# Performance work log

Hardware: AMD Instinct MI355X
Metric: run time of the kernel (lower is better)

The kernel has to match this reference:

```python
import jax, jax.numpy as jnp
import numpy as np
from jax import lax

G = 32          # growthrate / num_features
KS = 3          # filter_size
PAD = (KS - 1) // 2
NUM_LAYERS = 4


def _conv2d(x, w, b):
    # x: [B, Cin, H, W], w: [Cout, Cin, k, k]
    y = lax.conv_general_dilated(
        x, w, window_strides=(1, 1), padding=[(PAD, PAD), (PAD, PAD)],
        dimension_numbers=("NCHW", "OIHW", "NCHW"))
    return y + b[None, :, None, None]


def _scan_cell(xs, w, b):
    # xs: [T, B, Cin, H, W]; ConvLSTM-like cell: A = tanh(conv(cat(x, c)))
    # split A -> (ai[G], af[G], ao[1]); h = ai; c_next = sigmoid(ao) * af
    T, B, _, H, W = xs.shape
    c0 = jnp.zeros((B, G, H, W), xs.dtype)

    def step(c, x):
        A = jnp.tanh(_conv2d(jnp.concatenate([x, c], axis=1), w, b))
        h = A[:, :G]
        cand = A[:, G:2 * G]
        gate = jax.nn.sigmoid(A[:, 2 * G:])
        c_next = gate * cand
        return c_next, (h, c_next, gate)

    _, (hs, cs, gs) = lax.scan(step, c0, xs)
    return hs, cs, gs  # each [T, B, G or 1, H, W]


def setup_inputs() -> dict:
    key = jax.random.key(0)
    ks = jax.random.split(key, 1 + 4 * NUM_LAYERS)
    T, B, C, H, W = 8, 4, 32, 64, 64
    inp = {"x": jax.random.normal(ks[0], (T, B, C, H, W), jnp.float32)}
    cin = [C] + [2 * l * G for l in range(1, NUM_LAYERS)]  # [32, 64, 128, 192]
    cout = 2 * G + 1
    for l in range(NUM_LAYERS):
        ci = cin[l] + G
        inp[f"wf{l}"] = jax.random.normal(ks[1 + 4 * l], (cout, ci, KS, KS), jnp.float32) * 0.02
        inp[f"bf{l}"] = jax.random.normal(ks[2 + 4 * l], (cout,), jnp.float32) * 0.02
        inp[f"wb{l}"] = jax.random.normal(ks[3 + 4 * l], (cout, ci, KS, KS), jnp.float32) * 0.02
        inp[f"bb{l}"] = jax.random.normal(ks[4 + 4 * l], (cout,), jnp.float32) * 0.02
    return inp


def reference(x, wf0, bf0, wb0, bb0, wf1, bf1, wb1, bb1,
              wf2, bf2, wb2, bb2, wf3, bf3, wb3, bb3):
    fwd = [(wf0, bf0), (wf1, bf1), (wf2, bf2), (wf3, bf3)]
    bwd = [(wb0, bb0), (wb1, bb1), (wb2, bb2), (wb3, bb3)]
    output = x  # [T, B, C, H, W]
    lr_h, lr_c, lr_g = [], [], []
    for l in range(NUM_LAYERS):
        hf, cf, gf = _scan_cell(output, *fwd[l])
        hb, _, _ = _scan_cell(output[::-1], *bwd[l])
        hb = hb[::-1]  # align backward pass to original time order
        cur = jnp.concatenate([hf, hb], axis=2)  # [T, B, 2G, H, W]
        output = cur if l == 0 else jnp.concatenate([output, cur], axis=2)
        lr_h.append(hf[-1]); lr_c.append(cf[-1]); lr_g.append(gf[-1])
    return (output, jnp.stack(lr_h), jnp.stack(lr_c), jnp.stack(lr_g))
```

## Files before the change

### kernel.cpp

```cpp
#include <hip/hip_runtime.h>
#include <math.h>

#define T_STEPS 8
#define HW 4096
#define XSTR 192
#define FR_ROW 4352

typedef unsigned short u16;
typedef __attribute__((ext_vector_type(8))) short short8;
typedef __attribute__((ext_vector_type(4))) short short4v;
typedef __attribute__((ext_vector_type(4))) float f32x4;

__device__ __forceinline__ u16 f2bf(float f) {
    unsigned u = __builtin_bit_cast(unsigned, f);
    u += 0x7fffu + ((u >> 16) & 1u);
    return (u16)(u >> 16);
}
__device__ __forceinline__ float bf2f(u16 h) {
    unsigned u = ((unsigned)h) << 16;
    return __builtin_bit_cast(float, u);
}
__device__ __forceinline__ float ftanh(float x) {
    float e = __expf(2.f * x);
    return 1.f - 2.f * __builtin_amdgcn_rcpf(e + 1.f);
}
__device__ __forceinline__ float fsigm(float x) {
    return __builtin_amdgcn_rcpf(1.f + __expf(-x));
}

__global__ __launch_bounds__(256) void transpose_halo(
    const float* __restrict__ src, u16* __restrict__ XT, int src_ctot)
{
    __shared__ float tile[32][257];
    const int img = blockIdx.z;
    const int px0 = blockIdx.x * 256;
    const float* s = src + (size_t)img * src_ctot * HW + px0;
    #pragma unroll
    for (int c = 0; c < 32; ++c)
        tile[c][threadIdx.x] = s[(size_t)c * HW + threadIdx.x];
    __syncthreads();
    const int c = threadIdx.x & 31, pb = threadIdx.x >> 5;
    const int r0 = px0 >> 6;
    for (int p = pb; p < 256; p += 8) {
        int row = r0 + (p >> 6), col = p & 63;
        XT[((size_t)img * 4356 + (row + 1) * 66 + col + 1) * XSTR + c] = f2bf(tile[c][p]);
    }
}

__global__ __launch_bounds__(256) void prep_w(
    const float* __restrict__ wf, const float* __restrict__ wb,
    u16* __restrict__ Wr, int ci_total)
{
    int idx = blockIdx.x * 256 + threadIdx.x;
    int total = 2 * 9 * 80 * ci_total;
    if (idx >= total) return;
    int ci = idx % ci_total;
    int rest = idx / ci_total;
    int co = rest % 80; rest /= 80;
    int tap = rest % 9;
    int dir = rest / 9;
    const float* w = dir ? wb : wf;
    float v = (co < 65) ? w[((size_t)co * ci_total + ci) * 9 + tap] : 0.f;
    Wr[idx] = f2bf(v);
}

__global__ __launch_bounds__(512, 2) void convx_mfma(
    const u16* __restrict__ XT, const u16* __restrict__ Wr,
    const float* __restrict__ b_f, const float* __restrict__ b_b,
    u16* __restrict__ convx, int cin, int ci_total)
{
    __shared__ u16 xs[6 * 66 * 32];
    const int tid = threadIdx.x;
    const int l = tid & 63, wv = tid >> 6;
    const int g = l >> 4, ln16 = l & 15;
    const int img = blockIdx.z;
    const int dir = wv & 1;
    const int wrow = wv >> 1;
    const int r0  = blockIdx.x * 4;
    const int orow = r0 + wrow;

    const float* bias = dir ? b_b : b_f;
    f32x4 acc[5][4];
    #pragma unroll
    for (int mt = 0; mt < 5; ++mt)
        #pragma unroll
        for (int r = 0; r < 4; ++r) {
            int co = mt * 16 + g * 4 + r;
            float bv = (co < 65) ? bias[co] : 0.f;
            #pragma unroll
            for (int nt = 0; nt < 4; ++nt) acc[mt][nt][r] = bv;
        }

    const u16* wdir = Wr + (size_t)dir * 9 * 80 * ci_total + g * 8;
    const u16* xim  = XT + (size_t)img * 4356 * XSTR;

    for (int ch = 0; ch < cin; ch += 32) {
        __syncthreads();
        #pragma unroll
        for (int k = 0; k < 4; ++k) {
            int idx = k * 512 + tid;
            if (idx < 1584) {
                int seg = idx & 3;
                int pr  = idx >> 2;
                short8 v = *(const short8*)(xim + (size_t)(r0 * 66 + pr) * XSTR + ch + seg * 8);
                *(short8*)(xs + (size_t)idx * 8) = v;
            }
        }
        __syncthreads();

        #pragma unroll
        for (int ky = 0; ky < 3; ++ky) {
            #pragma unroll
            for (int kx = 0; kx < 3; ++kx) {
                const int tap = ky * 3 + kx;
                const u16* xb = xs + ((size_t)((wrow + ky) * 66 + ln16 + kx)) * 32 + g * 8;
                short8 bv0 = *(const short8*)(xb);
                short8 bv1 = *(const short8*)(xb + 16 * 32);
                short8 bv2 = *(const short8*)(xb + 32 * 32);
                short8 bv3 = *(const short8*)(xb + 48 * 32);
                const u16* wb_ = wdir + ((size_t)tap * 80 + ln16) * ci_total + ch;
                #pragma unroll
                for (int mt = 0; mt < 5; ++mt) {
                    short8 af = *(const short8*)(wb_ + (size_t)mt * 16 * ci_total);
                    acc[mt][0] = __builtin_amdgcn_mfma_f32_16x16x32_bf16(af, bv0, acc[mt][0], 0, 0, 0);
                    acc[mt][1] = __builtin_amdgcn_mfma_f32_16x16x32_bf16(af, bv1, acc[mt][1], 0, 0, 0);
                    acc[mt][2] = __builtin_amdgcn_mfma_f32_16x16x32_bf16(af, bv2, acc[mt][2], 0, 0, 0);
                    acc[mt][3] = __builtin_amdgcn_mfma_f32_16x16x32_bf16(af, bv3, acc[mt][3], 0, 0, 0);
                }
            }
        }
    }

    const int zimg = dir * 32 + img;
    u16* cb = convx + ((size_t)zimg * 64 + orow) * FR_ROW;
    #pragma unroll
    for (int mt = 0; mt < 4; ++mt)
        #pragma unroll
        for (int nt = 0; nt < 4; ++nt) {
            short4v pk;
            #pragma unroll
            for (int r = 0; r < 4; ++r) pk[r] = (short)f2bf(acc[mt][nt][r]);
            *(short4v*)(cb + (size_t)(nt * 4 + mt) * 256 + l * 4) = pk;
        }
    if (g == 0) {
        #pragma unroll
        for (int nt = 0; nt < 4; ++nt) {
            short4v pk;
            #pragma unroll
            for (int r = 0; r < 4; ++r) pk[r] = (short)f2bf(acc[4][nt][r]);
            *(short4v*)(cb + 4096 + nt * 64 + ln16 * 4) = pk;
        }
    }
}

__global__ __launch_bounds__(256) void rec_mfma(
    const u16* __restrict__ cT_in, u16* __restrict__ cT_out,
    const u16* __restrict__ Wr, const u16* __restrict__ convx,
    float* __restrict__ out_t,
    float* __restrict__ lrh, float* __restrict__ lrc, float* __restrict__ lrg,
    u16* __restrict__ XT,
    int cin, int ci_total, int layer, int step)
{
    const int tid = threadIdx.x;
    const int l = tid & 63, wv = tid >> 6;
    const int g = l >> 4, ln16 = l & 15;
    const int z = blockIdx.z;
    const int dir = z >> 2, b = z & 3;
    const int t = dir ? (7 - step) : step;
    const int row  = blockIdx.x * 2 + (wv >> 1);
    const int nb   = (wv & 1) * 2;
    const int col0 = nb * 16;

    const int zimg = dir * 32 + t * 4 + b;
    const u16* cxb = convx + ((size_t)zimg * 64 + row) * FR_ROW;
    f32x4 acc[5][2];
    #pragma unroll
    for (int mt = 0; mt < 4; ++mt)
        #pragma unroll
        for (int nt = 0; nt < 2; ++nt) {
            short4v pk = *(const short4v*)(cxb + (size_t)((nb + nt) * 4 + mt) * 256 + l * 4);
            #pragma unroll
            for (int r = 0; r < 4; ++r) acc[mt][nt][r] = bf2f((u16)pk[r]);
        }
    #pragma unroll
    for (int nt = 0; nt < 2; ++nt) {
        if (g == 0) {
            short4v pk = *(const short4v*)(cxb + 4096 + (nb + nt) * 64 + ln16 * 4);
            #pragma unroll
            for (int r = 0; r < 4; ++r) acc[4][nt][r] = bf2f((u16)pk[r]);
        } else {
            #pragma unroll
            for (int r = 0; r < 4; ++r) acc[4][nt][r] = 0.f;
        }
    }

    const u16* wdir = Wr + (size_t)dir * 9 * 80 * ci_total + cin + g * 8;
    const u16* cim  = cT_in + (size_t)z * 4356 * 32 + g * 8;

    #pragma unroll
    for (int ky = 0; ky < 3; ++ky) {
        #pragma unroll
        for (int kx = 0; kx < 3; ++kx) {
            const int tap = ky * 3 + kx;
            const u16* xb_ = cim + (size_t)((row + ky) * 66 + col0 + ln16 + kx) * 32;
            short8 bv0 = *(const short8*)(xb_);
            short8 bv1 = *(const short8*)(xb_ + 16 * 32);
            const u16* wb_ = wdir + ((size_t)tap * 80 + ln16) * ci_total;
            #pragma unroll
            for (int mt = 0; mt < 5; ++mt) {
                short8 af = *(const short8*)(wb_ + (size_t)mt * 16 * ci_total);
                acc[mt][0] = __builtin_amdgcn_mfma_f32_16x16x32_bf16(af, bv0, acc[mt][0], 0, 0, 0);
                acc[mt][1] = __builtin_amdgcn_mfma_f32_16x16x32_bf16(af, bv1, acc[mt][1], 0, 0, 0);
            }
        }
    }

    const bool last_f = (dir == 0) && (step == 7);
    float val[2], gv[2];
    #pragma unroll
    for (int nt = 0; nt < 2; ++nt) {
        val[nt] = fsigm(ftanh(acc[4][nt][0]));
        gv[nt]  = __shfl(val[nt], ln16);
    }

    const size_t obase = (size_t)(t * 4 + b) * 256 + 64 * layer + dir * 32;
    const int chb = 64 * layer + dir * 32;
    #pragma unroll
    for (int mt = 0; mt < 2; ++mt)
        #pragma unroll
        for (int nt = 0; nt < 2; ++nt) {
            int px = row * 64 + col0 + nt * 16 + ln16;
            short4v pkh;
            #pragma unroll
            for (int r = 0; r < 4; ++r) {
                int co = mt * 16 + g * 4 + r;
                float v = ftanh(acc[mt][nt][r]);
                out_t[(obase + co) * HW + px] = v;
                pkh[r] = (short)f2bf(v);
                if (last_f) lrh[((size_t)(layer * 4 + b) * 32 + co) * HW + px] = v;
            }
            if (layer < 3)
                *(short4v*)(XT + ((size_t)(t * 4 + b) * 4356 + (row + 1) * 66 +
                                  (col0 + nt * 16 + ln16 + 1)) * XSTR + chb + mt * 16 + g * 4) = pkh;
        }
    #pragma unroll
    for (int mt = 2; mt < 4; ++mt)
        #pragma unroll
        for (int nt = 0; nt < 2; ++nt) {
            short4v pk;
            #pragma unroll
            for (int r = 0; r < 4; ++r) {
                int k = (mt - 2) * 16 + g * 4 + r;
                float c = gv[nt] * ftanh(acc[mt][nt][r]);
                pk[r] = (short)f2bf(c);
                if (last_f)
                    lrc[((size_t)(layer * 4 + b) * 32 + k) * HW + row * 64 + col0 + nt * 16 + ln16] = c;
            }
            int colh = col0 + nt * 16 + ln16 + 1;
            *(short4v*)(cT_out + ((size_t)z * 4356 + (row + 1) * 66 + colh) * 32 + (mt - 2) * 16 + g * 4) = pk;
        }
    if (last_f && g == 0) {
        #pragma unroll
        for (int nt = 0; nt < 2; ++nt)
            lrg[(size_t)(layer * 4 + b) * HW + row * 64 + col0 + nt * 16 + ln16] = val[nt];
    }
}

extern "C" void kernel_launch(void* const* d_in, const int* in_sizes, int n_in,
                              void* d_out, int out_size, void* d_ws, size_t ws_size,
                              hipStream_t stream)
{
    const float* x = (const float*)d_in[0];
    float* out = (float*)d_out;
    float* lrh = out + (size_t)33554432;
    float* lrc = lrh + (size_t)2097152;
    float* lrg = lrc + (size_t)2097152;

    char* ws = (char*)d_ws;
    u16* convx = (u16*)ws;
    size_t off = 35651584 + 4096;
    u16* cT_a = (u16*)(ws + off); off += 2230272;
    u16* cT_b = (u16*)(ws + off); off += 2230272;
    u16* XT   = (u16*)(ws + off); off += 53526528;
    u16* Wr   = (u16*)(ws + off);

    hipMemsetAsync(XT, 0, 53526528, stream);
    hipMemsetAsync(cT_b, 0, 2230272, stream);
    transpose_halo<<<dim3(16, 1, 32), 256, 0, stream>>>(x, XT, 32);

    for (int l = 0; l < 4; ++l) {
        const float* wf = (const float*)d_in[1 + 4 * l];
        const float* bf = (const float*)d_in[2 + 4 * l];
        const float* wb = (const float*)d_in[3 + 4 * l];
        const float* bb = (const float*)d_in[4 + 4 * l];
        int cin = (l == 0) ? 32 : 64 * l;
        int ci_total = cin + 32;

        prep_w<<<dim3((2 * 9 * 80 * ci_total + 255) / 256), 256, 0, stream>>>(wf, wb, Wr, ci_total);
        convx_mfma<<<dim3(16, 1, 32), 512, 0, stream>>>(XT, Wr, bf, bb, convx, cin, ci_total);

        hipMemsetAsync(cT_a, 0, 2230272, stream);
        for (int s = 0; s < 8; ++s) {
            const u16* cin_p = (s & 1) ? cT_b : cT_a;
            u16* cout_p      = (s & 1) ? cT_a : cT_b;
            rec_mfma<<<dim3(32, 1, 8), 256, 0, stream>>>(
                cin_p, cout_p, Wr, convx, out, lrh, lrc, lrg, XT, cin, ci_total, l, s);
        }
    }
}
```

Measured before the change: 616.4 us.

## Fuse two recurrent timesteps per launch with halo recompute and async LDS staging

The recurrent kernel now runs two consecutive timesteps per launch. The first step is computed for the block's rows plus one halo row on each side, and its cell state is kept in shared memory for the second step. This halves the number of serial recurrent launches and cuts a global round trip of the cell state, in exchange for redundant halo-row computation and larger blocks. The input convolution also switches to double-buffered direct global-to-LDS loads so the next channel chunk is fetched while the current one feeds MFMA, which drops one barrier per chunk.

```diff
diff --git a/kernel.cpp b/kernel.cpp
--- a/kernel.cpp
+++ b/kernel.cpp
@@ -26,6 +26,11 @@
 }
 __device__ __forceinline__ float fsigm(float x) {
     return __builtin_amdgcn_rcpf(1.f + __expf(-x));
+}
+__device__ __forceinline__ void gload_lds16(const u16* g, u16* lds) {
+    __builtin_amdgcn_global_load_lds(
+        (const __attribute__((address_space(1))) unsigned*)g,
+        (__attribute__((address_space(3))) unsigned*)lds, 16, 0, 0);
 }
 
 __global__ __launch_bounds__(256) void transpose_halo(
@@ -69,7 +74,7 @@
     const float* __restrict__ b_f, const float* __restrict__ b_b,
     u16* __restrict__ convx, int cin, int ci_total)
 {
-    __shared__ u16 xs[6 * 66 * 32];
+    __shared__ u16 xs[2][16384];
     const int tid = threadIdx.x;
     const int l = tid & 63, wv = tid >> 6;
     const int g = l >> 4, ln16 = l & 15;
@@ -94,31 +99,35 @@
     const u16* wdir = Wr + (size_t)dir * 9 * 80 * ci_total + g * 8;
     const u16* xim  = XT + (size_t)img * 4356 * XSTR;
 
-    for (int ch = 0; ch < cin; ch += 32) {
+#define STAGE(buf, chv)                                                         \
+    {                                                                           \
+        _Pragma("unroll")                                                       \
+        for (int k = 0; k < 4; ++k) {                                           \
+            int idx = k * 512 + tid;                                            \
+            if (idx < 1584)                                                     \
+                gload_lds16(xim + (size_t)(r0 * 66 + (idx >> 2)) * XSTR + (chv) \
+                            + (idx & 3) * 8,                                    \
+                            &xs[buf][(size_t)idx * 8]);                         \
+        }                                                                       \
+    }
+
+    const int nch = cin >> 5;
+    int cur = 0;
+    STAGE(0, 0)
+    for (int ch = 0; ch < nch; ++ch) {
         __syncthreads();
-        #pragma unroll
-        for (int k = 0; k < 4; ++k) {
-            int idx = k * 512 + tid;
-            if (idx < 1584) {
-                int seg = idx & 3;
-                int pr  = idx >> 2;
-                short8 v = *(const short8*)(xim + (size_t)(r0 * 66 + pr) * XSTR + ch + seg * 8);
-                *(short8*)(xs + (size_t)idx * 8) = v;
-            }
-        }
-        __syncthreads();
-
+        if (ch + 1 < nch) STAGE(cur ^ 1, (ch + 1) * 32)
         #pragma unroll
         for (int ky = 0; ky < 3; ++ky) {
             #pragma unroll
             for (int kx = 0; kx < 3; ++kx) {
                 const int tap = ky * 3 + kx;
-                const u16* xb = xs + ((size_t)((wrow + ky) * 66 + ln16 + kx)) * 32 + g * 8;
+                const u16* xb = xs[cur] + ((size_t)((wrow + ky) * 66 + ln16 + kx)) * 32 + g * 8;
                 short8 bv0 = *(const short8*)(xb);
                 short8 bv1 = *(const short8*)(xb + 16 * 32);
                 short8 bv2 = *(const short8*)(xb + 32 * 32);
                 short8 bv3 = *(const short8*)(xb + 48 * 32);
-                const u16* wb_ = wdir + ((size_t)tap * 80 + ln16) * ci_total + ch;
+                const u16* wb_ = wdir + ((size_t)tap * 80 + ln16) * ci_total + ch * 32;
                 #pragma unroll
                 for (int mt = 0; mt < 5; ++mt) {
                     short8 af = *(const short8*)(wb_ + (size_t)mt * 16 * ci_total);
@@ -129,7 +138,9 @@
                 }
             }
         }
-    }
+        cur ^= 1;
+    }
+#undef STAGE
 
     const int zimg = dir * 32 + img;
     u16* cb = convx + ((size_t)zimg * 64 + orow) * FR_ROW;
@@ -153,116 +164,219 @@
     }
 }
 
-__global__ __launch_bounds__(256) void rec_mfma(
+__global__ __launch_bounds__(512) void rec2_mfma(
     const u16* __restrict__ cT_in, u16* __restrict__ cT_out,
     const u16* __restrict__ Wr, const u16* __restrict__ convx,
     float* __restrict__ out_t,
     float* __restrict__ lrh, float* __restrict__ lrc, float* __restrict__ lrg,
     u16* __restrict__ XT,
-    int cin, int ci_total, int layer, int step)
+    int cin, int ci_total, int layer, int s0)
 {
+    __shared__ u16 cls[4 * 4 * 66 * 8];
     const int tid = threadIdx.x;
-    const int l = tid & 63, wv = tid >> 6;
+    const int l = tid & 63, w = tid >> 6;
     const int g = l >> 4, ln16 = l & 15;
+    const int rb = blockIdx.x;
     const int z = blockIdx.z;
     const int dir = z >> 2, b = z & 3;
-    const int t = dir ? (7 - step) : step;
-    const int row  = blockIdx.x * 2 + (wv >> 1);
-    const int nb   = (wv & 1) * 2;
+    const int hf = w & 1;
+    const int nb = hf * 2;
     const int col0 = nb * 16;
-
-    const int zimg = dir * 32 + t * 4 + b;
-    const u16* cxb = convx + ((size_t)zimg * 64 + row) * FR_ROW;
-    f32x4 acc[5][2];
-    #pragma unroll
-    for (int mt = 0; mt < 4; ++mt)
+    const int row0 = rb * 2;
+
+    for (int i = tid; i < 8448; i += 512) cls[i] = 0;
+    __syncthreads();
+
+    const u16* wdir = Wr + (size_t)dir * 9 * 80 * ci_total + cin + g * 8;
+
+    {
+        const int rowA = row0 + (w >> 1) - 1;
+        const int lrA  = w >> 1;
+        if ((unsigned)rowA < 64u) {
+            const int t = dir ? (7 - s0) : s0;
+            const int zimg = dir * 32 + t * 4 + b;
+            const u16* cxb = convx + ((size_t)zimg * 64 + rowA) * FR_ROW;
+            f32x4 acc[5][2];
+            #pragma unroll
+            for (int mt = 0; mt < 4; ++mt)
+                #pragma unroll
+                for (int nt = 0; nt < 2; ++nt) {
+                    short4v pk = *(const short4v*)(cxb + (size_t)((nb + nt) * 4 + mt) * 256 + l * 4);
+                    #pragma unroll
+                    for (int r = 0; r < 4; ++r) acc[mt][nt][r] = bf2f((u16)pk[r]);
+                }
+            #pragma unroll
+            for (int nt = 0; nt < 2; ++nt) {
+                if (g == 0) {
+                    short4v pk = *(const short4v*)(cxb + 4096 + (nb + nt) * 64 + ln16 * 4);
+                    #pragma unroll
+                    for (int r = 0; r < 4; ++r) acc[4][nt][r] = bf2f((u16)pk[r]);
+                } else {
+                    #pragma unroll
+                    for (int r = 0; r < 4; ++r) acc[4][nt][r] = 0.f;
+                }
+            }
+
+            const u16* cim = cT_in + (size_t)z * 4356 * 32 + g * 8;
+            #pragma unroll
+            for (int ky = 0; ky < 3; ++ky) {
+                #pragma unroll
+                for (int kx = 0; kx < 3; ++kx) {
+                    const int tap = ky * 3 + kx;
+                    const u16* xb_ = cim + (size_t)((rowA + ky) * 66 + col0 + ln16 + kx) * 32;
+                    short8 bv0 = *(const short8*)(xb_);
+                    short8 bv1 = *(const short8*)(xb_ + 16 * 32);
+                    #pragma unroll
+                    for (int mt = 0; mt < 5; ++mt) {
+                        short8 af = *(const short8*)(wdir + ((size_t)tap * 80 + ln16) * ci_total
+                                                     + (size_t)mt * 16 * ci_total);
+                        acc[mt][0] = __builtin_amdgcn_mfma_f32_16x16x32_bf16(af, bv0, acc[mt][0], 0, 0, 0);
+                        acc[mt][1] = __builtin_amdgcn_mfma_f32_16x16x32_bf16(af, bv1, acc[mt][1], 0, 0, 0);
+                    }
+                }
+            }
+
+            float val[2], gv[2];
+            #pragma unroll
+            for (int nt = 0; nt < 2; ++nt) {
+                val[nt] = fsigm(ftanh(acc[4][nt][0]));
+                gv[nt]  = __shfl(val[nt], ln16);
+            }
+
+            const bool owned = (rowA >= row0) && (rowA < row0 + 2);
+            if (owned) {
+                const size_t obase = (size_t)(t * 4 + b) * 256 + 64 * layer + dir * 32;
+                const int chb = 64 * layer + dir * 32;
+                #pragma unroll
+                for (int mt = 0; mt < 2; ++mt)
+                    #pragma unroll
+                    for (int nt = 0; nt < 2; ++nt) {
+                        int px = rowA * 64 + col0 + nt * 16 + ln16;
+                        short4v pkh;
+                        #pragma unroll
+                        for (int r = 0; r < 4; ++r) {
+                            int co = mt * 16 + g * 4 + r;
+                            float v = ftanh(acc[mt][nt][r]);
+                            out_t[(obase + co) * HW + px] = v;
+                            pkh[r] = (short)f2bf(v);
+                        }
+                        if (layer < 3)
+                            *(short4v*)(XT + ((size_t)(t * 4 + b) * 4356 + (rowA + 1) * 66 +
+                                              (col0 + nt * 16 + ln16 + 1)) * XSTR + chb + mt * 16 + g * 4) = pkh;
+                    }
+            }
+            #pragma unroll
+            for (int mt = 2; mt < 4; ++mt)
+                #pragma unroll
+                for (int nt = 0; nt < 2; ++nt) {
+                    short4v pk;
+                    #pragma unroll
+                    for (int r = 0; r < 4; ++r)
+                        pk[r] = (short)f2bf(gv[nt] * ftanh(acc[mt][nt][r]));
+                    int colh = col0 + nt * 16 + ln16 + 1;
+                    int J = (mt - 2) * 2 + (g >> 1);
+                    *(short4v*)(cls + ((size_t)((J * 4 + lrA) * 66 + colh)) * 8 + (g & 1) * 4) = pk;
+                }
+        }
+    }
+    __syncthreads();
+
+    if (w < 4) {
+        const int s1 = s0 + 1;
+        const int rowB = row0 + (w >> 1);
+        const int t = dir ? (7 - s1) : s1;
+        const int zimg = dir * 32 + t * 4 + b;
+        const u16* cxb = convx + ((size_t)zimg * 64 + rowB) * FR_ROW;
+        f32x4 acc[5][2];
+        #pragma unroll
+        for (int mt = 0; mt < 4; ++mt)
+            #pragma unroll
+            for (int nt = 0; nt < 2; ++nt) {
+                short4v pk = *(const short4v*)(cxb + (size_t)((nb + nt) * 4 + mt) * 256 + l * 4);
+                #pragma unroll
+                for (int r = 0; r < 4; ++r) acc[mt][nt][r] = bf2f((u16)pk[r]);
+            }
         #pragma unroll
         for (int nt = 0; nt < 2; ++nt) {
-            short4v pk = *(const short4v*)(cxb + (size_t)((nb + nt) * 4 + mt) * 256 + l * 4);
-            #pragma unroll
-            for (int r = 0; r < 4; ++r) acc[mt][nt][r] = bf2f((u16)pk[r]);
-        }
-    #pragma unroll
-    for (int nt = 0; nt < 2; ++nt) {
-        if (g == 0) {
-            short4v pk = *(const short4v*)(cxb + 4096 + (nb + nt) * 64 + ln16 * 4);
-            #pragma unroll
-            for (int r = 0; r < 4; ++r) acc[4][nt][r] = bf2f((u16)pk[r]);
-        } else {
-            #pragma unroll
-            for (int r = 0; r < 4; ++r) acc[4][nt][r] = 0.f;
-        }
-    }
-
-    const u16* wdir = Wr + (size_t)dir * 9 * 80 * ci_total + cin + g * 8;
-    const u16* cim  = cT_in + (size_t)z * 4356 * 32 + g * 8;
-
-    #pragma unroll
-    for (int ky = 0; ky < 3; ++ky) {
-        #pragma unroll
-        for (int kx = 0; kx < 3; ++kx) {
-            const int tap = ky * 3 + kx;
-            const u16* xb_ = cim + (size_t)((row + ky) * 66 + col0 + ln16 + kx) * 32;
-            short8 bv0 = *(const short8*)(xb_);
-            short8 bv1 = *(const short8*)(xb_ + 16 * 32);
-            const u16* wb_ = wdir + ((size_t)tap * 80 + ln16) * ci_total;
-            #pragma unroll
-            for (int mt = 0; mt < 5; ++mt) {
-                short8 af = *(const short8*)(wb_ + (size_t)mt * 16 * ci_total);
-                acc[mt][0] = __builtin_amdgcn_mfma_f32_16x16x32_bf16(af, bv0, acc[mt][0], 0, 0, 0);
-                acc[mt][1] = __builtin_amdgcn_mfma_f32_16x16x32_bf16(af, bv1, acc[mt][1], 0, 0, 0);
-            }
-        }
-    }
-
-    const bool last_f = (dir == 0) && (step == 7);
-    float val[2], gv[2];
-    #pragma unroll
-    for (int nt = 0; nt < 2; ++nt) {
-        val[nt] = fsigm(ftanh(acc[4][nt][0]));
-        gv[nt]  = __shfl(val[nt], ln16);
-    }
-
-    const size_t obase = (size_t)(t * 4 + b) * 256 + 64 * layer + dir * 32;
-    const int chb = 64 * layer + dir * 32;
-    #pragma unroll
-    for (int mt = 0; mt < 2; ++mt)
+            if (g == 0) {
+                short4v pk = *(const short4v*)(cxb + 4096 + (nb + nt) * 64 + ln16 * 4);
+                #pragma unroll
+                for (int r = 0; r < 4; ++r) acc[4][nt][r] = bf2f((u16)pk[r]);
+            } else {
+                #pragma unroll
+                for (int r = 0; r < 4; ++r) acc[4][nt][r] = 0.f;
+            }
+        }
+
+        #pragma unroll
+        for (int ky = 0; ky < 3; ++ky) {
+            #pragma unroll
+            for (int kx = 0; kx < 3; ++kx) {
+                const int tap = ky * 3 + kx;
+                const int lrB = (w >> 1) + ky;
+                const int colv = col0 + ln16 + kx;
+                const u16* xb_ = cls + ((size_t)((g * 4 + lrB) * 66 + colv)) * 8;
+                short8 bv0 = *(const short8*)(xb_);
+                short8 bv1 = *(const short8*)(xb_ + 128);
+                #pragma unroll
+                for (int mt = 0; mt < 5; ++mt) {
+                    short8 af = *(const short8*)(wdir + ((size_t)tap * 80 + ln16) * ci_total
+                                                 + (size_t)mt * 16 * ci_total);
+                    acc[mt][0] = __builtin_amdgcn_mfma_f32_16x16x32_bf16(af, bv0, acc[mt][0], 0, 0, 0);
+                    acc[mt][1] = __builtin_amdgcn_mfma_f32_16x16x32_bf16(af, bv1, acc[mt][1], 0, 0, 0);
+                }
+            }
+        }
+
+        const bool last_f = (dir == 0) && (s1 == 7);
+        float val[2], gv[2];
         #pragma unroll
         for (int nt = 0; nt < 2; ++nt) {
-            int px = row * 64 + col0 + nt * 16 + ln16;
-            short4v pkh;
-            #pragma unroll
-            for (int r = 0; r < 4; ++r) {
-                int co = mt * 16 + g * 4 + r;
-                float v = ftanh(acc[mt][nt][r]);
-                out_t[(obase + co) * HW + px] = v;
-                pkh[r] = (short)f2bf(v);
-                if (last_f) lrh[((size_t)(layer * 4 + b) * 32 + co) * HW + px] = v;
-            }
-            if (layer < 3)
-                *(short4v*)(XT + ((size_t)(t * 4 + b) * 4356 + (row + 1) * 66 +
-                                  (col0 + nt * 16 + ln16 + 1)) * XSTR + chb + mt * 16 + g * 4) = pkh;
-        }
-    #pragma unroll
-    for (int mt = 2; mt < 4; ++mt)
-        #pragma unroll
-        for (int nt = 0; nt < 2; ++nt) {
-            short4v pk;
-            #pragma unroll
-            for (int r = 0; r < 4; ++r) {
-                int k = (mt - 2) * 16 + g * 4 + r;
-                float c = gv[nt] * ftanh(acc[mt][nt][r]);
-                pk[r] = (short)f2bf(c);
-                if (last_f)
-                    lrc[((size_t)(layer * 4 + b) * 32 + k) * HW + row * 64 + col0 + nt * 16 + ln16] = c;
-            }
-            int colh = col0 + nt * 16 + ln16 + 1;
-            *(short4v*)(cT_out + ((size_t)z * 4356 + (row + 1) * 66 + colh) * 32 + (mt - 2) * 16 + g * 4) = pk;
-        }
-    if (last_f && g == 0) {
-        #pragma unroll
-        for (int nt = 0; nt < 2; ++nt)
-            lrg[(size_t)(layer * 4 + b) * HW + row * 64 + col0 + nt * 16 + ln16] = val[nt];
+            val[nt] = fsigm(ftanh(acc[4][nt][0]));
+            gv[nt]  = __shfl(val[nt], ln16);
+        }
+
+        const size_t obase = (size_t)(t * 4 + b) * 256 + 64 * layer + dir * 32;
+        const int chb = 64 * layer + dir * 32;
+        #pragma unroll
+        for (int mt = 0; mt < 2; ++mt)
+            #pragma unroll
+            for (int nt = 0; nt < 2; ++nt) {
+                int px = rowB * 64 + col0 + nt * 16 + ln16;
+                short4v pkh;
+                #pragma unroll
+                for (int r = 0; r < 4; ++r) {
+                    int co = mt * 16 + g * 4 + r;
+                    float v = ftanh(acc[mt][nt][r]);
+                    out_t[(obase + co) * HW + px] = v;
+                    pkh[r] = (short)f2bf(v);
+                    if (last_f) lrh[((size_t)(layer * 4 + b) * 32 + co) * HW + px] = v;
+                }
+                if (layer < 3)
+                    *(short4v*)(XT + ((size_t)(t * 4 + b) * 4356 + (rowB + 1) * 66 +
+                                      (col0 + nt * 16 + ln16 + 1)) * XSTR + chb + mt * 16 + g * 4) = pkh;
+            }
+        #pragma unroll
+        for (int mt = 2; mt < 4; ++mt)
+            #pragma unroll
+            for (int nt = 0; nt < 2; ++nt) {
+                short4v pk;
+                #pragma unroll
+                for (int r = 0; r < 4; ++r) {
+                    int k = (mt - 2) * 16 + g * 4 + r;
+                    float c = gv[nt] * ftanh(acc[mt][nt][r]);
+                    pk[r] = (short)f2bf(c);
+                    if (last_f)
+                        lrc[((size_t)(layer * 4 + b) * 32 + k) * HW + rowB * 64 + col0 + nt * 16 + ln16] = c;
+                }
+                int colh = col0 + nt * 16 + ln16 + 1;
+                *(short4v*)(cT_out + ((size_t)z * 4356 + (rowB + 1) * 66 + colh) * 32 + (mt - 2) * 16 + g * 4) = pk;
+            }
+        if (last_f && g == 0) {
+            #pragma unroll
+            for (int nt = 0; nt < 2; ++nt)
+                lrg[(size_t)(layer * 4 + b) * HW + rowB * 64 + col0 + nt * 16 + ln16] = val[nt];
+        }
     }
 }
 
@@ -279,13 +393,16 @@
     char* ws = (char*)d_ws;
     u16* convx = (u16*)ws;
     size_t off = 35651584 + 4096;
-    u16* cT_a = (u16*)(ws + off); off += 2230272;
-    u16* cT_b = (u16*)(ws + off); off += 2230272;
-    u16* XT   = (u16*)(ws + off); off += 53526528;
-    u16* Wr   = (u16*)(ws + off);
+    u16* cT[3];
+    cT[0] = (u16*)(ws + off); off += 2230272;
+    cT[1] = (u16*)(ws + off); off += 2230272;
+    cT[2] = (u16*)(ws + off); off += 2230272;
+    u16* XT = (u16*)(ws + off); off += 53526528;
+    u16* Wr = (u16*)(ws + off);
 
     hipMemsetAsync(XT, 0, 53526528, stream);
-    hipMemsetAsync(cT_b, 0, 2230272, stream);
+    hipMemsetAsync(cT[1], 0, 2230272, stream);
+    hipMemsetAsync(cT[2], 0, 2230272, stream);
     transpose_halo<<<dim3(16, 1, 32), 256, 0, stream>>>(x, XT, 32);
 
     for (int l = 0; l < 4; ++l) {
@@ -299,12 +416,11 @@
         prep_w<<<dim3((2 * 9 * 80 * ci_total + 255) / 256), 256, 0, stream>>>(wf, wb, Wr, ci_total);
         convx_mfma<<<dim3(16, 1, 32), 512, 0, stream>>>(XT, Wr, bf, bb, convx, cin, ci_total);
 
-        hipMemsetAsync(cT_a, 0, 2230272, stream);
-        for (int s = 0; s < 8; ++s) {
-            const u16* cin_p = (s & 1) ? cT_b : cT_a;
-            u16* cout_p      = (s & 1) ? cT_a : cT_b;
-            rec_mfma<<<dim3(32, 1, 8), 256, 0, stream>>>(
-                cin_p, cout_p, Wr, convx, out, lrh, lrc, lrg, XT, cin, ci_total, l, s);
-        }
-    }
-}
+        hipMemsetAsync(cT[0], 0, 2230272, stream);
+        for (int p = 0; p < 4; ++p) {
+            rec2_mfma<<<dim3(32, 1, 8), 512, 0, stream>>>(
+                cT[p % 3], cT[(p + 1) % 3], Wr, convx, out, lrh, lrc, lrg, XT,
+                cin, ci_total, l, 2 * p);
+        }
+    }
+}
```

After: 734.2 us. +19.1%, slower.

## Fuse eight recurrent steps into one kernel with halo recompute in LDS

Applied to the files above, without the earlier changes.

Replaces the eight per-step recurrent launches with a single kernel per layer. Each block owns two rows and recomputes a shrinking halo of neighbouring rows, so the cell state stays in double-buffered LDS and never makes a round trip through global memory. The four per-layer weight-prep launches are also merged into one upfront launch. This removes many launches and global syncs, at the cost of redundant MFMA work on halo rows (up to 16 rows per block at the first step) and higher LDS use per block.

```diff
diff --git a/kernel.cpp b/kernel.cpp
--- a/kernel.cpp
+++ b/kernel.cpp
@@ -47,19 +47,24 @@
     }
 }
 
-__global__ __launch_bounds__(256) void prep_w(
-    const float* __restrict__ wf, const float* __restrict__ wb,
-    u16* __restrict__ Wr, int ci_total)
+struct WP { const float* p[8]; };
+
+__global__ __launch_bounds__(256) void prep_w_all(WP wp, u16* __restrict__ Wr)
 {
     int idx = blockIdx.x * 256 + threadIdx.x;
-    int total = 2 * 9 * 80 * ci_total;
-    if (idx >= total) return;
-    int ci = idx % ci_total;
-    int rest = idx / ci_total;
+    if (idx >= 783360) return;
+    const int offs[5] = {0, 92160, 230400, 460800, 783360};
+    const int cit[4]  = {64, 96, 160, 224};
+    int lay = 0;
+    while (idx >= offs[lay + 1]) ++lay;
+    int li = idx - offs[lay];
+    int ci_total = cit[lay];
+    int ci = li % ci_total;
+    int rest = li / ci_total;
     int co = rest % 80; rest /= 80;
     int tap = rest % 9;
     int dir = rest / 9;
-    const float* w = dir ? wb : wf;
+    const float* w = wp.p[lay * 2 + dir];
     float v = (co < 65) ? w[((size_t)co * ci_total + ci) * 9 + tap] : 0.f;
     Wr[idx] = f2bf(v);
 }
@@ -153,116 +158,147 @@
     }
 }
 
-__global__ __launch_bounds__(256) void rec_mfma(
-    const u16* __restrict__ cT_in, u16* __restrict__ cT_out,
+__global__ __launch_bounds__(512, 2) void rec8_mfma(
     const u16* __restrict__ Wr, const u16* __restrict__ convx,
-    float* __restrict__ out_t,
-    float* __restrict__ lrh, float* __restrict__ lrc, float* __restrict__ lrg,
-    u16* __restrict__ XT,
-    int cin, int ci_total, int layer, int step)
-{
+    float* __restrict__ out_t, float* __restrict__ lrh,
+    float* __restrict__ lrc, float* __restrict__ lrg,
+    u16* __restrict__ XT, int cin, int ci_total, int layer)
+{
+    __shared__ u16 cls[2][4 * 16 * 66 * 8];
     const int tid = threadIdx.x;
-    const int l = tid & 63, wv = tid >> 6;
+    const int l = tid & 63, w = tid >> 6;
     const int g = l >> 4, ln16 = l & 15;
-    const int z = blockIdx.z;
+    const int bid = blockIdx.x;
+    const int rb = bid >> 3, z = bid & 7;
     const int dir = z >> 2, b = z & 3;
-    const int t = dir ? (7 - step) : step;
-    const int row  = blockIdx.x * 2 + (wv >> 1);
-    const int nb   = (wv & 1) * 2;
-    const int col0 = nb * 16;
-
-    const int zimg = dir * 32 + t * 4 + b;
-    const u16* cxb = convx + ((size_t)zimg * 64 + row) * FR_ROW;
-    f32x4 acc[5][2];
-    #pragma unroll
-    for (int mt = 0; mt < 4; ++mt)
-        #pragma unroll
-        for (int nt = 0; nt < 2; ++nt) {
-            short4v pk = *(const short4v*)(cxb + (size_t)((nb + nt) * 4 + mt) * 256 + l * 4);
-            #pragma unroll
-            for (int r = 0; r < 4; ++r) acc[mt][nt][r] = bf2f((u16)pk[r]);
-        }
-    #pragma unroll
-    for (int nt = 0; nt < 2; ++nt) {
-        if (g == 0) {
-            short4v pk = *(const short4v*)(cxb + 4096 + (nb + nt) * 64 + ln16 * 4);
-            #pragma unroll
-            for (int r = 0; r < 4; ++r) acc[4][nt][r] = bf2f((u16)pk[r]);
-        } else {
-            #pragma unroll
-            for (int r = 0; r < 4; ++r) acc[4][nt][r] = 0.f;
-        }
-    }
+    const int r0 = rb * 2;
+
+    {
+        short8 zz = {0, 0, 0, 0, 0, 0, 0, 0};
+        short8* f = (short8*)&cls[0][0];
+        for (int i = tid; i < 8448; i += 512) f[i] = zz;
+    }
+    __syncthreads();
 
     const u16* wdir = Wr + (size_t)dir * 9 * 80 * ci_total + cin + g * 8;
-    const u16* cim  = cT_in + (size_t)z * 4356 * 32 + g * 8;
-
-    #pragma unroll
-    for (int ky = 0; ky < 3; ++ky) {
-        #pragma unroll
-        for (int kx = 0; kx < 3; ++kx) {
-            const int tap = ky * 3 + kx;
-            const u16* xb_ = cim + (size_t)((row + ky) * 66 + col0 + ln16 + kx) * 32;
-            short8 bv0 = *(const short8*)(xb_);
-            short8 bv1 = *(const short8*)(xb_ + 16 * 32);
-            const u16* wb_ = wdir + ((size_t)tap * 80 + ln16) * ci_total;
-            #pragma unroll
-            for (int mt = 0; mt < 5; ++mt) {
-                short8 af = *(const short8*)(wb_ + (size_t)mt * 16 * ci_total);
-                acc[mt][0] = __builtin_amdgcn_mfma_f32_16x16x32_bf16(af, bv0, acc[mt][0], 0, 0, 0);
-                acc[mt][1] = __builtin_amdgcn_mfma_f32_16x16x32_bf16(af, bv1, acc[mt][1], 0, 0, 0);
-            }
-        }
-    }
-
-    const bool last_f = (dir == 0) && (step == 7);
-    float val[2], gv[2];
-    #pragma unroll
-    for (int nt = 0; nt < 2; ++nt) {
-        val[nt] = fsigm(ftanh(acc[4][nt][0]));
-        gv[nt]  = __shfl(val[nt], ln16);
-    }
-
-    const size_t obase = (size_t)(t * 4 + b) * 256 + 64 * layer + dir * 32;
-    const int chb = 64 * layer + dir * 32;
-    #pragma unroll
-    for (int mt = 0; mt < 2; ++mt)
-        #pragma unroll
-        for (int nt = 0; nt < 2; ++nt) {
-            int px = row * 64 + col0 + nt * 16 + ln16;
-            short4v pkh;
-            #pragma unroll
-            for (int r = 0; r < 4; ++r) {
-                int co = mt * 16 + g * 4 + r;
-                float v = ftanh(acc[mt][nt][r]);
-                out_t[(obase + co) * HW + px] = v;
-                pkh[r] = (short)f2bf(v);
-                if (last_f) lrh[((size_t)(layer * 4 + b) * 32 + co) * HW + px] = v;
-            }
-            if (layer < 3)
-                *(short4v*)(XT + ((size_t)(t * 4 + b) * 4356 + (row + 1) * 66 +
-                                  (col0 + nt * 16 + ln16 + 1)) * XSTR + chb + mt * 16 + g * 4) = pkh;
-        }
-    #pragma unroll
-    for (int mt = 2; mt < 4; ++mt)
-        #pragma unroll
-        for (int nt = 0; nt < 2; ++nt) {
-            short4v pk;
-            #pragma unroll
-            for (int r = 0; r < 4; ++r) {
-                int k = (mt - 2) * 16 + g * 4 + r;
-                float c = gv[nt] * ftanh(acc[mt][nt][r]);
-                pk[r] = (short)f2bf(c);
-                if (last_f)
-                    lrc[((size_t)(layer * 4 + b) * 32 + k) * HW + row * 64 + col0 + nt * 16 + ln16] = c;
-            }
-            int colh = col0 + nt * 16 + ln16 + 1;
-            *(short4v*)(cT_out + ((size_t)z * 4356 + (row + 1) * 66 + colh) * 32 + (mt - 2) * 16 + g * 4) = pk;
-        }
-    if (last_f && g == 0) {
-        #pragma unroll
-        for (int nt = 0; nt < 2; ++nt)
-            lrg[(size_t)(layer * 4 + b) * HW + row * 64 + col0 + nt * 16 + ln16] = val[nt];
+
+    #pragma unroll 1
+    for (int p = 0; p < 8; ++p) {
+        u16* wlds        = cls[p & 1];
+        const u16* rlds  = cls[(p & 1) ^ 1];
+        const int t = dir ? (7 - p) : p;
+        const int zimg = dir * 32 + t * 4 + b;
+        const int rlo = r0 - 7 + p;
+        const int ntasks = (16 - 2 * p) * 2;
+        const bool last_f = (dir == 0) && (p == 7);
+
+        #pragma unroll 1
+        for (int task = w; task < ntasks; task += 8) {
+            const int rowA = rlo + (task >> 1);
+            if ((unsigned)rowA >= 64u) continue;
+            const int nb2 = (task & 1) * 2;
+            const int col0 = nb2 * 16;
+
+            const u16* cxb = convx + ((size_t)zimg * 64 + rowA) * FR_ROW;
+            f32x4 acc[5][2];
+            #pragma unroll
+            for (int mt = 0; mt < 4; ++mt)
+                #pragma unroll
+                for (int nt = 0; nt < 2; ++nt) {
+                    short4v pk = *(const short4v*)(cxb + (size_t)((nb2 + nt) * 4 + mt) * 256 + l * 4);
+                    #pragma unroll
+                    for (int r = 0; r < 4; ++r) acc[mt][nt][r] = bf2f((u16)pk[r]);
+                }
+            #pragma unroll
+            for (int nt = 0; nt < 2; ++nt) {
+                if (g == 0) {
+                    short4v pk = *(const short4v*)(cxb + 4096 + (nb2 + nt) * 64 + ln16 * 4);
+                    #pragma unroll
+                    for (int r = 0; r < 4; ++r) acc[4][nt][r] = bf2f((u16)pk[r]);
+                } else {
+                    #pragma unroll
+                    for (int r = 0; r < 4; ++r) acc[4][nt][r] = 0.f;
+                }
+            }
+
+            if (p > 0) {
+                #pragma unroll
+                for (int ky = 0; ky < 3; ++ky) {
+                    #pragma unroll
+                    for (int kx = 0; kx < 3; ++kx) {
+                        const int tap = ky * 3 + kx;
+                        const int lr = rowA - r0 + 6 + ky;
+                        const int colv = col0 + ln16 + kx;
+                        const u16* xb_ = rlds + ((size_t)((g * 16 + lr) * 66 + colv)) * 8;
+                        short8 bv0 = *(const short8*)(xb_);
+                        short8 bv1 = *(const short8*)(xb_ + 128);
+                        #pragma unroll
+                        for (int mt = 0; mt < 5; ++mt) {
+                            short8 af = *(const short8*)(wdir + ((size_t)tap * 80 + ln16) * ci_total
+                                                         + (size_t)mt * 16 * ci_total);
+                            acc[mt][0] = __builtin_amdgcn_mfma_f32_16x16x32_bf16(af, bv0, acc[mt][0], 0, 0, 0);
+                            acc[mt][1] = __builtin_amdgcn_mfma_f32_16x16x32_bf16(af, bv1, acc[mt][1], 0, 0, 0);
+                        }
+                    }
+                }
+            }
+
+            float val[2], gv[2];
+            #pragma unroll
+            for (int nt = 0; nt < 2; ++nt) {
+                val[nt] = fsigm(ftanh(acc[4][nt][0]));
+                gv[nt]  = __shfl(val[nt], ln16);
+            }
+
+            const bool owned = (rowA >= r0) && (rowA < r0 + 2);
+            if (owned) {
+                const size_t obase = (size_t)(t * 4 + b) * 256 + 64 * layer + dir * 32;
+                const int chb = 64 * layer + dir * 32;
+                #pragma unroll
+                for (int mt = 0; mt < 2; ++mt)
+                    #pragma unroll
+                    for (int nt = 0; nt < 2; ++nt) {
+                        int px = rowA * 64 + col0 + nt * 16 + ln16;
+                        short4v pkh;
+                        #pragma unroll
+                        for (int r = 0; r < 4; ++r) {
+                            int co = mt * 16 + g * 4 + r;
+                            float v = ftanh(acc[mt][nt][r]);
+                            out_t[(obase + co) * HW + px] = v;
+                            pkh[r] = (short)f2bf(v);
+                            if (last_f) lrh[((size_t)(layer * 4 + b) * 32 + co) * HW + px] = v;
+                        }
+                        if (layer < 3)
+                            *(short4v*)(XT + ((size_t)(t * 4 + b) * 4356 + (rowA + 1) * 66 +
+                                              (col0 + nt * 16 + ln16 + 1)) * XSTR + chb + mt * 16 + g * 4) = pkh;
+                    }
+                if (last_f && g == 0) {
+                    #pragma unroll
+                    for (int nt = 0; nt < 2; ++nt)
+                        lrg[(size_t)(layer * 4 + b) * HW + rowA * 64 + col0 + nt * 16 + ln16] = val[nt];
+                }
+            }
+
+            const int lrW = rowA - r0 + 7;
+            #pragma unroll
+            for (int mt = 2; mt < 4; ++mt)
+                #pragma unroll
+                for (int nt = 0; nt < 2; ++nt) {
+                    short4v pk;
+                    #pragma unroll
+                    for (int r = 0; r < 4; ++r) {
+                        int k = (mt - 2) * 16 + g * 4 + r;
+                        float cval = gv[nt] * ftanh(acc[mt][nt][r]);
+                        pk[r] = (short)f2bf(cval);
+                        if (last_f && owned)
+                            lrc[((size_t)(layer * 4 + b) * 32 + k) * HW + rowA * 64 + col0 + nt * 16 + ln16] = cval;
+                    }
+                    int colh = col0 + nt * 16 + ln16 + 1;
+                    int J = (mt - 2) * 2 + (g >> 1);
+                    *(short4v*)(wlds + ((size_t)((J * 16 + lrW) * 66 + colh)) * 8 + (g & 1) * 4) = pk;
+                }
+        }
+        __syncthreads();
     }
 }
 
@@ -279,32 +315,30 @@
     char* ws = (char*)d_ws;
     u16* convx = (u16*)ws;
     size_t off = 35651584 + 4096;
-    u16* cT_a = (u16*)(ws + off); off += 2230272;
-    u16* cT_b = (u16*)(ws + off); off += 2230272;
-    u16* XT   = (u16*)(ws + off); off += 53526528;
-    u16* Wr   = (u16*)(ws + off);
+    u16* XT = (u16*)(ws + off); off += 53526528;
+    u16* Wr = (u16*)(ws + off);
+
+    static const int offs[4] = {0, 92160, 230400, 460800};
 
     hipMemsetAsync(XT, 0, 53526528, stream);
-    hipMemsetAsync(cT_b, 0, 2230272, stream);
     transpose_halo<<<dim3(16, 1, 32), 256, 0, stream>>>(x, XT, 32);
 
+    WP wp;
     for (int l = 0; l < 4; ++l) {
-        const float* wf = (const float*)d_in[1 + 4 * l];
+        wp.p[l * 2]     = (const float*)d_in[1 + 4 * l];
+        wp.p[l * 2 + 1] = (const float*)d_in[3 + 4 * l];
+    }
+    prep_w_all<<<dim3((783360 + 255) / 256), 256, 0, stream>>>(wp, Wr);
+
+    for (int l = 0; l < 4; ++l) {
         const float* bf = (const float*)d_in[2 + 4 * l];
-        const float* wb = (const float*)d_in[3 + 4 * l];
         const float* bb = (const float*)d_in[4 + 4 * l];
         int cin = (l == 0) ? 32 : 64 * l;
         int ci_total = cin + 32;
-
-        prep_w<<<dim3((2 * 9 * 80 * ci_total + 255) / 256), 256, 0, stream>>>(wf, wb, Wr, ci_total);
-        convx_mfma<<<dim3(16, 1, 32), 512, 0, stream>>>(XT, Wr, bf, bb, convx, cin, ci_total);
-
-        hipMemsetAsync(cT_a, 0, 2230272, stream);
-        for (int s = 0; s < 8; ++s) {
-            const u16* cin_p = (s & 1) ? cT_b : cT_a;
-            u16* cout_p      = (s & 1) ? cT_a : cT_b;
-            rec_mfma<<<dim3(32, 1, 8), 256, 0, stream>>>(
-                cin_p, cout_p, Wr, convx, out, lrh, lrc, lrg, XT, cin, ci_total, l, s);
-        }
-    }
-}
+        const u16* Wrl = Wr + offs[l];
+
+        convx_mfma<<<dim3(16, 1, 32), 512, 0, stream>>>(XT, Wrl, bf, bb, convx, cin, ci_total);
+        rec8_mfma<<<dim3(256), 512, 0, stream>>>(
+            Wrl, convx, out, lrh, lrc, lrg, XT, cin, ci_total, l);
+    }
+}
```

Result: slower. 771.0 us (+25.1%).

## Split conv and recurrent kernels into smaller tiles, swizzle LDS, batch weight prep

Applied to the files above, without the earlier changes.

The input-conv kernel now gives each wave half a row (2 rows per block, double the grid), uses a swizzled segment-major LDS layout to cut bank conflicts, and raises the occupancy hint. The recurrent step kernel now handles one row per block, with each wave covering 16 columns, which doubles the grid and halves per-wave accumulators to spread the small per-step work over more CUs. Weight prep for all four layers is merged into a single launch ahead of the layer loop, removing per-layer launches. In exchange, weights are reloaded more often per output, and LDS staging is repeated for more blocks with less halo reuse.

```diff
diff --git a/kernel.cpp b/kernel.cpp
--- a/kernel.cpp
+++ b/kernel.cpp
@@ -47,40 +47,47 @@
     }
 }
 
-__global__ __launch_bounds__(256) void prep_w(
-    const float* __restrict__ wf, const float* __restrict__ wb,
-    u16* __restrict__ Wr, int ci_total)
+struct WP { const float* p[8]; };
+
+__global__ __launch_bounds__(256) void prep_w_all(WP wp, u16* __restrict__ Wr)
 {
     int idx = blockIdx.x * 256 + threadIdx.x;
-    int total = 2 * 9 * 80 * ci_total;
-    if (idx >= total) return;
-    int ci = idx % ci_total;
-    int rest = idx / ci_total;
+    if (idx >= 783360) return;
+    const int offs[5] = {0, 92160, 230400, 460800, 783360};
+    const int cit[4]  = {64, 96, 160, 224};
+    int lay = 0;
+    while (idx >= offs[lay + 1]) ++lay;
+    int li = idx - offs[lay];
+    int ci_total = cit[lay];
+    int ci = li % ci_total;
+    int rest = li / ci_total;
     int co = rest % 80; rest /= 80;
     int tap = rest % 9;
     int dir = rest / 9;
-    const float* w = dir ? wb : wf;
+    const float* w = wp.p[lay * 2 + dir];
     float v = (co < 65) ? w[((size_t)co * ci_total + ci) * 9 + tap] : 0.f;
     Wr[idx] = f2bf(v);
 }
 
-__global__ __launch_bounds__(512, 2) void convx_mfma(
+__global__ __launch_bounds__(512, 6) void convx_mfma(
     const u16* __restrict__ XT, const u16* __restrict__ Wr,
     const float* __restrict__ b_f, const float* __restrict__ b_b,
     u16* __restrict__ convx, int cin, int ci_total)
 {
-    __shared__ u16 xs[6 * 66 * 32];
+    __shared__ u16 xs[4 * 264 * 8];
     const int tid = threadIdx.x;
     const int l = tid & 63, wv = tid >> 6;
     const int g = l >> 4, ln16 = l & 15;
     const int img = blockIdx.z;
-    const int dir = wv & 1;
-    const int wrow = wv >> 1;
-    const int r0  = blockIdx.x * 4;
+    const int dir  = wv & 1;
+    const int half = (wv >> 1) & 1;
+    const int wrow = wv >> 2;
+    const int r0  = blockIdx.x * 2;
     const int orow = r0 + wrow;
+    const int col0 = half * 32;
 
     const float* bias = dir ? b_b : b_f;
-    f32x4 acc[5][4];
+    f32x4 acc[5][2];
     #pragma unroll
     for (int mt = 0; mt < 5; ++mt)
         #pragma unroll
@@ -88,7 +95,7 @@
             int co = mt * 16 + g * 4 + r;
             float bv = (co < 65) ? bias[co] : 0.f;
             #pragma unroll
-            for (int nt = 0; nt < 4; ++nt) acc[mt][nt][r] = bv;
+            for (int nt = 0; nt < 2; ++nt) acc[mt][nt][r] = bv;
         }
 
     const u16* wdir = Wr + (size_t)dir * 9 * 80 * ci_total + g * 8;
@@ -97,13 +104,12 @@
     for (int ch = 0; ch < cin; ch += 32) {
         __syncthreads();
         #pragma unroll
-        for (int k = 0; k < 4; ++k) {
+        for (int k = 0; k < 3; ++k) {
             int idx = k * 512 + tid;
-            if (idx < 1584) {
-                int seg = idx & 3;
-                int pr  = idx >> 2;
+            if (idx < 1056) {
+                int seg = idx & 3, pr = idx >> 2;
                 short8 v = *(const short8*)(xim + (size_t)(r0 * 66 + pr) * XSTR + ch + seg * 8);
-                *(short8*)(xs + (size_t)idx * 8) = v;
+                *(short8*)(xs + (size_t)(seg * 264 + (pr ^ (seg << 1))) * 8) = v;
             }
         }
         __syncthreads();
@@ -113,19 +119,16 @@
             #pragma unroll
             for (int kx = 0; kx < 3; ++kx) {
                 const int tap = ky * 3 + kx;
-                const u16* xb = xs + ((size_t)((wrow + ky) * 66 + ln16 + kx)) * 32 + g * 8;
+                const int px0 = (wrow + ky) * 66 + col0 + ln16 + kx;
+                const u16* xb = xs + (size_t)(g * 264 + (px0 ^ (g << 1))) * 8;
                 short8 bv0 = *(const short8*)(xb);
-                short8 bv1 = *(const short8*)(xb + 16 * 32);
-                short8 bv2 = *(const short8*)(xb + 32 * 32);
-                short8 bv3 = *(const short8*)(xb + 48 * 32);
+                short8 bv1 = *(const short8*)(xb + 128);
                 const u16* wb_ = wdir + ((size_t)tap * 80 + ln16) * ci_total + ch;
                 #pragma unroll
                 for (int mt = 0; mt < 5; ++mt) {
                     short8 af = *(const short8*)(wb_ + (size_t)mt * 16 * ci_total);
                     acc[mt][0] = __builtin_amdgcn_mfma_f32_16x16x32_bf16(af, bv0, acc[mt][0], 0, 0, 0);
                     acc[mt][1] = __builtin_amdgcn_mfma_f32_16x16x32_bf16(af, bv1, acc[mt][1], 0, 0, 0);
-                    acc[mt][2] = __builtin_amdgcn_mfma_f32_16x16x32_bf16(af, bv2, acc[mt][2], 0, 0, 0);
-                    acc[mt][3] = __builtin_amdgcn_mfma_f32_16x16x32_bf16(af, bv3, acc[mt][3], 0, 0, 0);
                 }
             }
         }
@@ -136,19 +139,21 @@
     #pragma unroll
     for (int mt = 0; mt < 4; ++mt)
         #pragma unroll
-        for (int nt = 0; nt < 4; ++nt) {
+        for (int nt = 0; nt < 2; ++nt) {
+            int NT = half * 2 + nt;
             short4v pk;
             #pragma unroll
             for (int r = 0; r < 4; ++r) pk[r] = (short)f2bf(acc[mt][nt][r]);
-            *(short4v*)(cb + (size_t)(nt * 4 + mt) * 256 + l * 4) = pk;
+            *(short4v*)(cb + (size_t)(NT * 4 + mt) * 256 + l * 4) = pk;
         }
     if (g == 0) {
         #pragma unroll
-        for (int nt = 0; nt < 4; ++nt) {
+        for (int nt = 0; nt < 2; ++nt) {
+            int NT = half * 2 + nt;
             short4v pk;
             #pragma unroll
             for (int r = 0; r < 4; ++r) pk[r] = (short)f2bf(acc[4][nt][r]);
-            *(short4v*)(cb + 4096 + nt * 64 + ln16 * 4) = pk;
+            *(short4v*)(cb + 4096 + NT * 64 + ln16 * 4) = pk;
         }
     }
 }
@@ -162,36 +167,30 @@
     int cin, int ci_total, int layer, int step)
 {
     const int tid = threadIdx.x;
-    const int l = tid & 63, wv = tid >> 6;
+    const int l = tid & 63, q = tid >> 6;
     const int g = l >> 4, ln16 = l & 15;
+    const int row = blockIdx.x;
     const int z = blockIdx.z;
     const int dir = z >> 2, b = z & 3;
     const int t = dir ? (7 - step) : step;
-    const int row  = blockIdx.x * 2 + (wv >> 1);
-    const int nb   = (wv & 1) * 2;
-    const int col0 = nb * 16;
-
+    const int col0 = q * 16;
     const int zimg = dir * 32 + t * 4 + b;
+
     const u16* cxb = convx + ((size_t)zimg * 64 + row) * FR_ROW;
-    f32x4 acc[5][2];
-    #pragma unroll
-    for (int mt = 0; mt < 4; ++mt)
-        #pragma unroll
-        for (int nt = 0; nt < 2; ++nt) {
-            short4v pk = *(const short4v*)(cxb + (size_t)((nb + nt) * 4 + mt) * 256 + l * 4);
-            #pragma unroll
-            for (int r = 0; r < 4; ++r) acc[mt][nt][r] = bf2f((u16)pk[r]);
-        }
-    #pragma unroll
-    for (int nt = 0; nt < 2; ++nt) {
-        if (g == 0) {
-            short4v pk = *(const short4v*)(cxb + 4096 + (nb + nt) * 64 + ln16 * 4);
-            #pragma unroll
-            for (int r = 0; r < 4; ++r) acc[4][nt][r] = bf2f((u16)pk[r]);
-        } else {
-            #pragma unroll
-            for (int r = 0; r < 4; ++r) acc[4][nt][r] = 0.f;
-        }
+    f32x4 acc[5];
+    #pragma unroll
+    for (int mt = 0; mt < 4; ++mt) {
+        short4v pk = *(const short4v*)(cxb + (size_t)(q * 4 + mt) * 256 + l * 4);
+        #pragma unroll
+        for (int r = 0; r < 4; ++r) acc[mt][r] = bf2f((u16)pk[r]);
+    }
+    if (g == 0) {
+        short4v pk = *(const short4v*)(cxb + 4096 + q * 64 + ln16 * 4);
+        #pragma unroll
+        for (int r = 0; r < 4; ++r) acc[4][r] = bf2f((u16)pk[r]);
+    } else {
+        #pragma unroll
+        for (int r = 0; r < 4; ++r) acc[4][r] = 0.f;
     }
 
     const u16* wdir = Wr + (size_t)dir * 9 * 80 * ci_total + cin + g * 8;
@@ -203,67 +202,54 @@
         for (int kx = 0; kx < 3; ++kx) {
             const int tap = ky * 3 + kx;
             const u16* xb_ = cim + (size_t)((row + ky) * 66 + col0 + ln16 + kx) * 32;
-            short8 bv0 = *(const short8*)(xb_);
-            short8 bv1 = *(const short8*)(xb_ + 16 * 32);
+            short8 bv = *(const short8*)(xb_);
             const u16* wb_ = wdir + ((size_t)tap * 80 + ln16) * ci_total;
             #pragma unroll
             for (int mt = 0; mt < 5; ++mt) {
                 short8 af = *(const short8*)(wb_ + (size_t)mt * 16 * ci_total);
-                acc[mt][0] = __builtin_amdgcn_mfma_f32_16x16x32_bf16(af, bv0, acc[mt][0], 0, 0, 0);
-                acc[mt][1] = __builtin_amdgcn_mfma_f32_16x16x32_bf16(af, bv1, acc[mt][1], 0, 0, 0);
+                acc[mt] = __builtin_amdgcn_mfma_f32_16x16x32_bf16(af, bv, acc[mt], 0, 0, 0);
             }
         }
     }
 
     const bool last_f = (dir == 0) && (step == 7);
-    float val[2], gv[2];
-    #pragma unroll
-    for (int nt = 0; nt < 2; ++nt) {
-        val[nt] = fsigm(ftanh(acc[4][nt][0]));
-        gv[nt]  = __shfl(val[nt], ln16);
-    }
+    float val = fsigm(ftanh(acc[4][0]));
+    float gv  = __shfl(val, ln16);
 
     const size_t obase = (size_t)(t * 4 + b) * 256 + 64 * layer + dir * 32;
     const int chb = 64 * layer + dir * 32;
-    #pragma unroll
-    for (int mt = 0; mt < 2; ++mt)
-        #pragma unroll
-        for (int nt = 0; nt < 2; ++nt) {
-            int px = row * 64 + col0 + nt * 16 + ln16;
-            short4v pkh;
-            #pragma unroll
-            for (int r = 0; r < 4; ++r) {
-                int co = mt * 16 + g * 4 + r;
-                float v = ftanh(acc[mt][nt][r]);
-                out_t[(obase + co) * HW + px] = v;
-                pkh[r] = (short)f2bf(v);
-                if (last_f) lrh[((size_t)(layer * 4 + b) * 32 + co) * HW + px] = v;
-            }
-            if (layer < 3)
-                *(short4v*)(XT + ((size_t)(t * 4 + b) * 4356 + (row + 1) * 66 +
-                                  (col0 + nt * 16 + ln16 + 1)) * XSTR + chb + mt * 16 + g * 4) = pkh;
-        }
-    #pragma unroll
-    for (int mt = 2; mt < 4; ++mt)
-        #pragma unroll
-        for (int nt = 0; nt < 2; ++nt) {
-            short4v pk;
-            #pragma unroll
-            for (int r = 0; r < 4; ++r) {
-                int k = (mt - 2) * 16 + g * 4 + r;
-                float c = gv[nt] * ftanh(acc[mt][nt][r]);
-                pk[r] = (short)f2bf(c);
-                if (last_f)
-                    lrc[((size_t)(layer * 4 + b) * 32 + k) * HW + row * 64 + col0 + nt * 16 + ln16] = c;
-            }
-            int colh = col0 + nt * 16 + ln16 + 1;
-            *(short4v*)(cT_out + ((size_t)z * 4356 + (row + 1) * 66 + colh) * 32 + (mt - 2) * 16 + g * 4) = pk;
-        }
-    if (last_f && g == 0) {
-        #pragma unroll
-        for (int nt = 0; nt < 2; ++nt)
-            lrg[(size_t)(layer * 4 + b) * HW + row * 64 + col0 + nt * 16 + ln16] = val[nt];
-    }
+    const int px = row * 64 + col0 + ln16;
+    #pragma unroll
+    for (int mt = 0; mt < 2; ++mt) {
+        short4v pkh;
+        #pragma unroll
+        for (int r = 0; r < 4; ++r) {
+            int co = mt * 16 + g * 4 + r;
+            float v = ftanh(acc[mt][r]);
+            out_t[(obase + co) * HW + px] = v;
+            pkh[r] = (short)f2bf(v);
+            if (last_f) lrh[((size_t)(layer * 4 + b) * 32 + co) * HW + px] = v;
+        }
+        if (layer < 3)
+            *(short4v*)(XT + ((size_t)(t * 4 + b) * 4356 + (row + 1) * 66 +
+                              (col0 + ln16 + 1)) * XSTR + chb + mt * 16 + g * 4) = pkh;
+    }
+    #pragma unroll
+    for (int mt = 2; mt < 4; ++mt) {
+        short4v pk;
+        #pragma unroll
+        for (int r = 0; r < 4; ++r) {
+            int k = (mt - 2) * 16 + g * 4 + r;
+            float c = gv * ftanh(acc[mt][r]);
+            pk[r] = (short)f2bf(c);
+            if (last_f)
+                lrc[((size_t)(layer * 4 + b) * 32 + k) * HW + px] = c;
+        }
+        *(short4v*)(cT_out + ((size_t)z * 4356 + (row + 1) * 66 +
+                              (col0 + ln16 + 1)) * 32 + (mt - 2) * 16 + g * 4) = pk;
+    }
+    if (last_f && g == 0)
+        lrg[(size_t)(layer * 4 + b) * HW + px] = val;
 }
 
 extern "C" void kernel_launch(void* const* d_in, const int* in_sizes, int n_in,
@@ -281,30 +267,38 @@
     size_t off = 35651584 + 4096;
     u16* cT_a = (u16*)(ws + off); off += 2230272;
     u16* cT_b = (u16*)(ws + off); off += 2230272;
-    u16* XT   = (u16*)(ws + off); off += 53526528;
-    u16* Wr   = (u16*)(ws + off);
+    u16* XT = (u16*)(ws + off); off += 53526528;
+    u16* Wr = (u16*)(ws + off);
+
+    static const int offs[4] = {0, 92160, 230400, 460800};
 
     hipMemsetAsync(XT, 0, 53526528, stream);
     hipMemsetAsync(cT_b, 0, 2230272, stream);
     transpose_halo<<<dim3(16, 1, 32), 256, 0, stream>>>(x, XT, 32);
 
+    WP wp;
     for (int l = 0; l < 4; ++l) {
-        const float* wf = (const float*)d_in[1 + 4 * l];
+        wp.p[l * 2]     = (const float*)d_in[1 + 4 * l];
+        wp.p[l * 2 + 1] = (const float*)d_in[3 + 4 * l];
+    }
+    prep_w_all<<<dim3((783360 + 255) / 256), 256, 0, stream>>>(wp, Wr);
+
+    for (int l = 0; l < 4; ++l) {
         const float* bf = (const float*)d_in[2 + 4 * l];
-        const float* wb = (const float*)d_in[3 + 4 * l];
         const float* bb = (const float*)d_in[4 + 4 * l];
         int cin = (l == 0) ? 32 : 64 * l;
         int ci_total = cin + 32;
-
-        prep_w<<<dim3((2 * 9 * 80 * ci_total + 255) / 256), 256, 0, stream>>>(wf, wb, Wr, ci_total);
-        convx_mfma<<<dim3(16, 1, 32), 512, 0, stream>>>(XT, Wr, bf, bb, convx, cin, ci_total);
+        const u16* Wrl = Wr + offs[l];
+
+        convx_mfma<<<dim3(32, 1, 32), 512, 0, stream>>>(XT, Wrl, bf, bb, convx, cin, ci_total);
 
         hipMemsetAsync(cT_a, 0, 2230272, stream);
         for (int s = 0; s < 8; ++s) {
             const u16* cin_p = (s & 1) ? cT_b : cT_a;
             u16* cout_p      = (s & 1) ? cT_a : cT_b;
-            rec_mfma<<<dim3(32, 1, 8), 256, 0, stream>>>(
-                cin_p, cout_p, Wr, convx, out, lrh, lrc, lrg, XT, cin, ci_total, l, s);
-        }
-    }
-}
+            rec_mfma<<<dim3(64, 1, 8), 256, 0, stream>>>(
+                cin_p, cout_p, Wrl, convx, out, lrh, lrc, lrg, XT,
+                cin, ci_total, l, s);
+        }
+    }
+}
```

After: 873.5 us. 41.7% more time.
